# Performance work log

Hardware: AMD Instinct MI355X
Metric: run time of the kernel (lower is better)

Reference implementation:

```python
import jax, jax.numpy as jnp
import numpy as np

B, CH, H, W = 32, 128, 32, 32
EMB = 64      # embedding_dim
NEMB = 8192   # codebook size


def setup_inputs() -> dict:
    key = jax.random.key(0)
    k1, k2, k3, k4 = jax.random.split(key, 4)
    z = jax.random.normal(k1, (B, CH, H, W), jnp.float32)
    # 1x1 conv == per-pixel linear: weight [EMB, CH], bias [EMB]
    proj_w = jax.random.normal(k2, (EMB, CH), jnp.float32) * 0.05
    proj_b = jax.random.normal(k3, (EMB,), jnp.float32) * 0.01
    embed_w = jax.random.normal(k4, (NEMB, EMB), jnp.float32)
    return {"z": z, "proj_w": proj_w, "proj_b": proj_b, "embed_w": embed_w}


def reference(z, proj_w, proj_b, embed_w):
    Bz, C, Hh, Ww = z.shape
    sg = jax.lax.stop_gradient
    # 1x1 conv then permute(0,2,3,1): [B,C,H,W] -> [B,H,W,E]
    z_e = jnp.einsum('bchw,ec->bhwe', z, proj_w) + proj_b
    flat = z_e.reshape(-1, z_e.shape[-1])  # [N, E], N = B*H*W
    dist = ((flat * flat).sum(1, keepdims=True)
            - 2.0 * (flat @ embed_w.T)
            + (embed_w * embed_w).sum(1)[None, :])
    z_q_ind = jnp.argmin(dist, axis=1).reshape(Bz, Hh, Ww)  # argmax(-dist)
    z_q_emb = embed_w[z_q_ind]  # gather: [B,H,W,E]
    commitment_cost = 0.25
    kld_scale = 10.0
    latent_loss = kld_scale * (
        commitment_cost * jnp.mean((sg(z_q_emb) - z_e) ** 2)
        + jnp.mean((z_q_emb - sg(z_e)) ** 2))
    z_q_flat = z_q_emb
    # straight-through estimator
    z_q_st = z_e + sg(z_q_emb - z_e)
    out = jnp.transpose(z_q_st, (0, 3, 1, 2))  # [B,E,H,W]
    return out, z_q_flat, latent_loss, z_q_ind
```

## Files before the change

### kernel.cpp

```cpp
#include <hip/hip_runtime.h>

#define NPIX   32768
#define NEMB_  8192
#define EMB_   64
#define CH_    128
#define CAPP   512

#define OUT_OFF  0
#define ZQ_OFF   2097152
#define LOSS_OFF 4194304
#define IND_OFF  4194305

typedef _Float16 h8   __attribute__((ext_vector_type(8)));
typedef float    f16f __attribute__((ext_vector_type(16)));

__global__ __launch_bounds__(256) void k_wpack(
    const float* __restrict__ ew, float4* __restrict__ W4,
    float* __restrict__ wsq, float* __restrict__ wsqp,
    float* __restrict__ lacc, int* __restrict__ done)
{
    const int tid = threadIdx.x;
    const int m   = blockIdx.x * 256 + tid;
    const float4* wr = (const float4*)(ew + (size_t)m * EMB_);
    float w[EMB_];
    float s = 0.f;
    #pragma unroll
    for (int i = 0; i < 16; i++) {
        float4 v = wr[i];
        w[4*i] = v.x; w[4*i+1] = v.y; w[4*i+2] = v.z; w[4*i+3] = v.w;
        s += v.x*v.x + v.y*v.y + v.z*v.z + v.w*v.w;
    }
    wsq[m] = s;
    float sh = (float)(_Float16)s;
    float sl = s - sh;
    const int t  = m >> 5;
    const int li = m & 31;
    #pragma unroll
    for (int s5 = 0; s5 < 4; s5++) {
        #pragma unroll
        for (int h = 0; h < 2; h++) {
            h8 hh;
            #pragma unroll
            for (int j = 0; j < 8; j++) hh[j] = (_Float16)w[s5 * 16 + h * 8 + j];
            W4[(size_t)(t * 5 + s5) * 64 + h * 32 + li] = __builtin_bit_cast(float4, hh);
        }
    }
    {
        h8 hh;
        #pragma unroll
        for (int j = 0; j < 8; j++) hh[j] = (_Float16)0.f;
        hh[0] = (_Float16)sh; hh[1] = (_Float16)sl;
        W4[(size_t)(t * 5 + 4) * 64 + 0 * 32 + li] = __builtin_bit_cast(float4, hh);
        #pragma unroll
        for (int j = 0; j < 8; j++) hh[j] = (_Float16)0.f;
        W4[(size_t)(t * 5 + 4) * 64 + 1 * 32 + li] = __builtin_bit_cast(float4, hh);
    }
    __shared__ float red[256];
    red[tid] = s;
    __syncthreads();
    for (int o = 128; o > 0; o >>= 1) {
        if (tid < o) red[tid] = fmaxf(red[tid], red[tid + o]);
        __syncthreads();
    }
    if (tid == 0) wsqp[blockIdx.x] = red[0];
    if (blockIdx.x == 0 && tid == 0) { *lacc = 0.f; *done = 0; }
}

__global__ __launch_bounds__(256) void k_proj(
    const float* __restrict__ z, const float* __restrict__ pw,
    const float* __restrict__ pb, float* __restrict__ z_e,
    float* __restrict__ xsq)
{
    __shared__ __align__(16) float wT[CH_ * EMB_];
    __shared__ float xp[4][64];
    const int tid = threadIdx.x;
    for (int i = tid; i < CH_ * EMB_; i += 256) {
        const int c = i >> 6, e = i & 63;
        wT[i] = pw[e * CH_ + c];
    }
    __syncthreads();

    const int px = tid & 63;
    const int eq = tid >> 6;
    const int n  = blockIdx.x * 64 + px;
    const int b  = n >> 10;
    const int hw = n & 1023;
    const float* zp = z + (size_t)b * (CH_ * 1024) + hw;

    float acc[16];
    #pragma unroll
    for (int j = 0; j < 16; j++) acc[j] = 0.f;

    #pragma unroll 4
    for (int c = 0; c < CH_; c++) {
        const float zv = zp[(size_t)c * 1024];
        const float4* wr = (const float4*)(wT + c * EMB_ + eq * 16);
        float4 w0 = wr[0], w1 = wr[1], w2 = wr[2], w3 = wr[3];
        acc[0]  = fmaf(zv, w0.x, acc[0]);  acc[1]  = fmaf(zv, w0.y, acc[1]);
        acc[2]  = fmaf(zv, w0.z, acc[2]);  acc[3]  = fmaf(zv, w0.w, acc[3]);
        acc[4]  = fmaf(zv, w1.x, acc[4]);  acc[5]  = fmaf(zv, w1.y, acc[5]);
        acc[6]  = fmaf(zv, w1.z, acc[6]);  acc[7]  = fmaf(zv, w1.w, acc[7]);
        acc[8]  = fmaf(zv, w2.x, acc[8]);  acc[9]  = fmaf(zv, w2.y, acc[9]);
        acc[10] = fmaf(zv, w2.z, acc[10]); acc[11] = fmaf(zv, w2.w, acc[11]);
        acc[12] = fmaf(zv, w3.x, acc[12]); acc[13] = fmaf(zv, w3.y, acc[13]);
        acc[14] = fmaf(zv, w3.z, acc[14]); acc[15] = fmaf(zv, w3.w, acc[15]);
    }

    const float4* pb4 = (const float4*)(pb + eq * 16);
    float4 b0 = pb4[0], b1 = pb4[1], b2 = pb4[2], b3 = pb4[3];
    float bb[16] = {b0.x,b0.y,b0.z,b0.w, b1.x,b1.y,b1.z,b1.w,
                    b2.x,b2.y,b2.z,b2.w, b3.x,b3.y,b3.z,b3.w};
    float sq = 0.f;
    #pragma unroll
    for (int j = 0; j < 16; j++) { acc[j] += bb[j]; sq += acc[j] * acc[j]; }

    float4* zo = (float4*)(z_e + (size_t)n * EMB_ + eq * 16);
    zo[0] = make_float4(acc[0],  acc[1],  acc[2],  acc[3]);
    zo[1] = make_float4(acc[4],  acc[5],  acc[6],  acc[7]);
    zo[2] = make_float4(acc[8],  acc[9],  acc[10], acc[11]);
    zo[3] = make_float4(acc[12], acc[13], acc[14], acc[15]);
    xp[eq][px] = sq;
    __syncthreads();
    if (tid < 64)
        xsq[blockIdx.x * 64 + tid] = xp[0][tid] + xp[1][tid] + xp[2][tid] + xp[3][tid];
}

__device__ __forceinline__ unsigned long long pack_key(float d, int m)
{
    unsigned fb = __float_as_uint(d);
    fb ^= ((int)fb < 0) ? 0xFFFFFFFFu : 0x80000000u;
    return ((unsigned long long)fb << 32) | (unsigned)m;
}

__global__ __launch_bounds__(256, 2) void k_fused2(
    const float4* __restrict__ W4, const float* __restrict__ z_e,
    const float* __restrict__ xsq, const float* __restrict__ wsqp,
    const float* __restrict__ wsq, const float* __restrict__ ew,
    float* __restrict__ out, float* __restrict__ lacc, int* __restrict__ done)
{
    __shared__ __align__(16) float xs[64][68];
    __shared__ float s1s[512], s2s[512], s3s[512];
    __shared__ short i1s[512], i2s[512];
    __shared__ float thr_s[64];
    __shared__ int   pairs[CAPP];
    __shared__ unsigned long long wbest[4][64];
    __shared__ int   winner_s[64];
    __shared__ int   smask[64];
    __shared__ float lred[256];
    __shared__ int   npair_s;
    __shared__ float wm_s;

    const int tid  = threadIdx.x;
    const int wv   = tid >> 6;
    const int lane = tid & 63;
    const int n0   = blockIdx.x * 64;
    const int hlf  = lane >> 5;

    if (tid == 0) npair_s = 0;
    if (tid < 64) smask[tid] = 0;
    wbest[wv][lane] = ~0ULL;
    if (tid < 32) {
        float w = wsqp[tid];
        #pragma unroll
        for (int o = 16; o > 0; o >>= 1) w = fmaxf(w, __shfl_xor(w, o));
        if (tid == 0) wm_s = w;
    }
    #pragma unroll
    for (int k = 0; k < 4; k++) {
        const int idx = k * 256 + tid;
        const int px = idx >> 4, i = idx & 15;
        ((float4*)&xs[px][0])[i] =
            *(const float4*)(z_e + (size_t)(n0 + px) * EMB_ + i * 4);
    }
    __syncthreads();

    h8 bfr[2][5];
    #pragma unroll
    for (int j = 0; j < 2; j++) {
        const int px = j * 32 + (lane & 31);
        #pragma unroll
        for (int s5 = 0; s5 < 4; s5++) {
            float4 u0 = *(const float4*)(&xs[px][s5 * 16 + hlf * 8]);
            float4 u1 = *(const float4*)(&xs[px][s5 * 16 + hlf * 8 + 4]);
            h8 hh;
            hh[0]=(_Float16)u0.x; hh[1]=(_Float16)u0.y; hh[2]=(_Float16)u0.z; hh[3]=(_Float16)u0.w;
            hh[4]=(_Float16)u1.x; hh[5]=(_Float16)u1.y; hh[6]=(_Float16)u1.z; hh[7]=(_Float16)u1.w;
            bfr[j][s5] = hh;
        }
        h8 hh;
        #pragma unroll
        for (int q = 0; q < 8; q++) hh[q] = (_Float16)0.f;
        if (hlf == 0) { hh[0] = (_Float16)-0.5f; hh[1] = (_Float16)-0.5f; }
        bfr[j][4] = hh;
    }

    const f16f kzero = {0,0,0,0,0,0,0,0,0,0,0,0,0,0,0,0};
    float s1[2], s2[2], s3[2];
    int   i1[2], i2[2];
    #pragma unroll
    for (int j = 0; j < 2; j++) { s1[j]=s2[j]=s3[j]=-3.0e38f; i1[j]=i2[j]=0; }

    const int tb = wv * 64;
    const float4* Wb = W4 + (size_t)tb * 320 + lane;
    float4 A0[5], A1[5];
    #pragma unroll
    for (int s = 0; s < 5; s++) A0[s] = Wb[s * 64];
    #pragma unroll
    for (int s = 0; s < 5; s++) A1[s] = Wb[320 + s * 64];

#define TILE_BODY(AB, TT, PF)                                                  \
    {                                                                          \
        const int gt = tb + (TT);                                              \
        f16f acc[2];                                                           \
        _Pragma("unroll")                                                      \
        for (int j = 0; j < 2; j++)                                            \
            acc[j] = __builtin_amdgcn_mfma_f32_32x32x16_f16(                   \
                __builtin_bit_cast(h8, AB[0]), bfr[j][0], kzero, 0, 0, 0);     \
        _Pragma("unroll")                                                      \
        for (int s = 1; s < 5; s++) {                                          \
            h8 a = __builtin_bit_cast(h8, AB[s]);                              \
            _Pragma("unroll")                                                  \
            for (int j = 0; j < 2; j++)                                        \
                acc[j] = __builtin_amdgcn_mfma_f32_32x32x16_f16(a, bfr[j][s],  \
                                                                acc[j],0,0,0); \
        }                                                                      \
        {                                                                      \
            const int tp = (PF) < 64 ? (PF) : 63;                              \
            const float4* wp = Wb + (size_t)tp * 320;                          \
            _Pragma("unroll")                                                  \
            for (int s = 0; s < 5; s++) AB[s] = wp[s * 64];                    \
        }                                                                      \
        _Pragma("unroll")                                                      \
        for (int j = 0; j < 2; j++) {                                          \
            float t0 = fmaxf(fmaxf(acc[j][0],  acc[j][1]),  acc[j][2]);        \
            float t1 = fmaxf(fmaxf(acc[j][3],  acc[j][4]),  acc[j][5]);        \
            float t2 = fmaxf(fmaxf(acc[j][6],  acc[j][7]),  acc[j][8]);        \
            float t3 = fmaxf(fmaxf(acc[j][9],  acc[j][10]), acc[j][11]);       \
            float t4 = fmaxf(fmaxf(acc[j][12], acc[j][13]), acc[j][14]);       \
            float v  = fmaxf(fmaxf(fmaxf(t0, t1), fmaxf(t2, t3)),              \
                             fmaxf(t4, acc[j][15]));                           \
            v = fmaxf(v, __shfl_xor(v, 32));                                   \
            bool c1 = v > s1[j];                                               \
            bool c2 = v > s2[j];                                               \
            int  cand = c1 ? i1[j] : gt;                                       \
            i2[j] = c2 ? cand : i2[j];                                         \
            s3[j] = fmaxf(fminf(s2[j], v), s3[j]);                             \
            s3[j] = fminf(s3[j], fmaxf(s2[j], v));                             \
            s2[j] = fmaxf(fminf(s1[j], v), fminf(s2[j], fmaxf(s1[j], v)));     \
            i1[j] = c1 ? gt : i1[j];                                           \
            s1[j] = fmaxf(s1[j], v);                                           \
        }                                                                      \
        if (((TT) & 31) == 31) {                                               \
            const int ch = (tb + (TT)) >> 5;                                   \
            if (lane < 32) {                                                   \
                _Pragma("unroll")                                              \
                for (int j = 0; j < 2; j++) {                                  \
                    const int cell = (j * 32 + lane) * 8 + ch;                 \
                    s1s[cell] = s1[j]; s2s[cell] = s2[j]; s3s[cell] = s3[j];   \
                    i1s[cell] = (short)i1[j]; i2s[cell] = (short)i2[j];        \
                }                                                              \
            }                                                                  \
            _Pragma("unroll")                                                  \
            for (int j = 0; j < 2; j++) {                                      \
                s1[j]=s2[j]=s3[j]=-3.0e38f; i1[j]=i2[j]=0;                     \
            }                                                                  \
        }                                                                      \
    }

    for (int tt = 0; tt < 64; tt += 2) {
        TILE_BODY(A0, tt,     tt + 2)
        TILE_BODY(A1, tt + 1, tt + 3)
    }
#undef TILE_BODY
    __syncthreads();

    if (tid < 64) {
        float s1g = s1s[tid * 8];
        #pragma unroll
        for (int c = 1; c < 8; c++) s1g = fmaxf(s1g, s1s[tid * 8 + c]);
        float E = 0.00125f * sqrtf(xsq[n0 + tid] * wm_s) + 1e-5f * wm_s + 3e-4f;
        thr_s[tid] = s1g - 2.0f * E;
    }
    __syncthreads();
    #pragma unroll
    for (int k = 0; k < 2; k++) {
        const int cell = k * 256 + tid;
        const int px = cell >> 3, ch = cell & 7;
        const float th = thr_s[px];
        const float cs1 = s1s[cell], cs2 = s2s[cell], cs3 = s3s[cell];
        if (cs3 >= th) {
            int pos = atomicAdd(&npair_s, 32);
            if (pos + 32 <= CAPP) {
                for (int t = 0; t < 32; t++)
                    pairs[pos + t] = (px << 8) | (ch * 32 + t);
            } else {
                for (int t = 0; t < 32; t++)
                    if (pos + t < CAPP) pairs[pos + t] = -1;
                smask[px] = 1;
            }
        } else {
            if (cs1 >= th) {
                int pos = atomicAdd(&npair_s, 1);
                if (pos < CAPP) pairs[pos] = (px << 8) | (int)i1s[cell];
                else smask[px] = 1;
            }
            if (cs2 >= th) {
                int pos = atomicAdd(&npair_s, 1);
                if (pos < CAPP) pairs[pos] = (px << 8) | (int)i2s[cell];
                else smask[px] = 1;
            }
        }
    }
    __syncthreads();
    const int np = npair_s < CAPP ? npair_s : CAPP;

    const int lg = lane >> 4;
    const int ld = lane & 15;
    for (int i = wv; i < np; i += 4) {
        const int pr = pairs[i];
        if (pr < 0) continue;
        const int p = pr >> 8;
        if (smask[p]) continue;
        const int t = pr & 255;
        const float4* tb4 = (const float4*)(ew + (size_t)t * 2048);
        float4 wq[8];
        #pragma unroll
        for (int q = 0; q < 8; q++) wq[q] = tb4[q * 64 + lane];
        const float4 xq = *(const float4*)(&xs[p][ld * 4]);
        unsigned long long best = ~0ULL;
        #pragma unroll
        for (int q = 0; q < 8; q++) {
            float dp = wq[q].x*xq.x + wq[q].y*xq.y + wq[q].z*xq.z + wq[q].w*xq.w;
            dp += __shfl_xor(dp, 1);
            dp += __shfl_xor(dp, 2);
            dp += __shfl_xor(dp, 4);
            dp += __shfl_xor(dp, 8);
            const int m = t * 32 + q * 4 + lg;
            unsigned long long key = pack_key(fmaf(-2.f, dp, wsq[m]), m);
            best = key < best ? key : best;
        }
        { unsigned long long o = __shfl_xor(best, 16); best = o < best ? o : best; }
        { unsigned long long o = __shfl_xor(best, 32); best = o < best ? o : best; }
        if (lane == 0) {
            unsigned long long cur = wbest[wv][p];
            wbest[wv][p] = best < cur ? best : cur;
        }
    }
    for (int p = wv; p < 64; p += 4) {
        if (!smask[p]) continue;
        const float4 xq = *(const float4*)(&xs[p][ld * 4]);
        unsigned long long bk = ~0ULL;
        for (int t = 0; t < 256; t++) {
            const float4* tb4 = (const float4*)(ew + (size_t)t * 2048);
            #pragma unroll
            for (int q = 0; q < 8; q++) {
                float4 wv4 = tb4[q * 64 + lane];
                float dp = wv4.x*xq.x + wv4.y*xq.y + wv4.z*xq.z + wv4.w*xq.w;
                dp += __shfl_xor(dp, 1);
                dp += __shfl_xor(dp, 2);
                dp += __shfl_xor(dp, 4);
                dp += __shfl_xor(dp, 8);
                const int m = t * 32 + q * 4 + lg;
                unsigned long long key = pack_key(fmaf(-2.f, dp, wsq[m]), m);
                bk = key < bk ? key : bk;
            }
        }
        { unsigned long long o = __shfl_xor(bk, 16); bk = o < bk ? o : bk; }
        { unsigned long long o = __shfl_xor(bk, 32); bk = o < bk ? o : bk; }
        if (lane == 0) {
            unsigned long long cur = wbest[wv][p];
            wbest[wv][p] = bk < cur ? bk : cur;
        }
    }
    __syncthreads();
    if (tid < 64) {
        unsigned long long k0 = wbest[0][tid];
        unsigned long long k1 = wbest[1][tid];
        unsigned long long k2 = wbest[2][tid];
        unsigned long long k3 = wbest[3][tid];
        k0 = k1 < k0 ? k1 : k0;
        k2 = k3 < k2 ? k3 : k2;
        k0 = k2 < k0 ? k2 : k0;
        const int win = (int)(unsigned)(k0 & 0xFFFFFFFFULL);
        winner_s[tid] = win;
        out[IND_OFF + n0 + tid] = (float)win;
    }
    __syncthreads();
    float lsum = 0.f;
    {
        const int px = tid >> 2, sg = tid & 3;
        const int win = winner_s[px];
        const float4* wr = (const float4*)(ew + (size_t)win * EMB_ + sg * 16);
        float4* xr  = (float4*)(&xs[px][sg * 16]);
        float4* zq4 = (float4*)(out + ZQ_OFF + (size_t)(n0 + px) * EMB_ + sg * 16);
        #pragma unroll
        for (int i = 0; i < 4; i++) {
            float4 w4v = wr[i];
            float4 z4  = xr[i];
            float d0 = w4v.x - z4.x, d1 = w4v.y - z4.y;
            float d2 = w4v.z - z4.z, d3 = w4v.w - z4.w;
            lsum += d0*d0 + d1*d1 + d2*d2 + d3*d3;
            xr[i]  = w4v;
            zq4[i] = w4v;
        }
    }
    __syncthreads();
    {
        const int bI  = n0 >> 10;
        const int hw0 = n0 & 1023;
        float* ob = out + OUT_OFF + (size_t)bI * (EMB_ * 1024) + hw0;
        #pragma unroll
        for (int r = 0; r < 16; r++) {
            const int idx = r * 256 + tid;
            const int e = idx >> 6, px = idx & 63;
            ob[(size_t)e * 1024 + px] = xs[px][e];
        }
    }
    lred[tid] = lsum;
    __syncthreads();
    for (int o = 128; o > 0; o >>= 1) {
        if (tid < o) lred[tid] += lred[tid + o];
        __syncthreads();
    }
    if (tid == 0) {
        atomicAdd(lacc, lred[0]);
        __threadfence();
        int old = atomicAdd(done, 1);
        if (old == (int)gridDim.x - 1) {
            float tot = atomicAdd(lacc, 0.0f);
            out[LOSS_OFF] = 12.5f * (tot / 2097152.0f);
        }
    }
}

extern "C" void kernel_launch(void* const* d_in, const int* in_sizes, int n_in,
                              void* d_out, int out_size, void* d_ws, size_t ws_size,
                              hipStream_t stream)
{
    const float* z  = (const float*)d_in[0];
    const float* pw = (const float*)d_in[1];
    const float* pb = (const float*)d_in[2];
    const float* ew = (const float*)d_in[3];
    float* out = (float*)d_out;

    char* ws = (char*)d_ws;
    float4* W4   = (float4*)(ws);
    float*  xsq  = (float*) (ws + 1310720);
    float*  wsq  = (float*) (ws + 1441792);
    float*  wsqp = (float*) (ws + 1474560);
    float*  lacc = (float*) (ws + 1474688);
    int*    done = (int*)   (ws + 1474692);

    float* z_e = out + ZQ_OFF;

    hipLaunchKernelGGL(k_wpack,  dim3(32),  dim3(256), 0, stream,
                       ew, W4, wsq, wsqp, lacc, done);
    hipLaunchKernelGGL(k_proj,   dim3(512), dim3(256), 0, stream,
                       z, pw, pb, z_e, xsq);
    hipLaunchKernelGGL(k_fused2, dim3(512), dim3(256), 0, stream,
                       W4, z_e, xsq, wsqp, wsq, ew, out, lacc, done);
}
```

Baseline: 186.6 us.

## Enlarge fused VQ tile to 128 pixels with 8 waves and pretransposed projection weights

The fused distance/argmin kernel now handles 128 pixels per block with 512 threads. Each wave covers 32 codebook tiles for 4 pixel groups, so every loaded codebook fragment feeds twice as many MFMAs and the per-chunk candidate flush happens once at the end. Per-pixel winners are merged with shared-memory atomicMin, and the loss reduction uses wave shuffles. The projection weight transpose moves into the codebook-pack kernel so k_proj reads pwT directly instead of rebuilding a shared transposed copy in every block. The trade-offs are higher register and LDS use, only 256 blocks (fewer waves to hide latency), and a larger candidate-pair buffer.

```diff
diff --git a/kernel.cpp b/kernel.cpp
--- a/kernel.cpp
+++ b/kernel.cpp
@@ -4,7 +4,7 @@
 #define NEMB_  8192
 #define EMB_   64
 #define CH_    128
-#define CAPP   512
+#define CAPP   768
 
 #define OUT_OFF  0
 #define ZQ_OFF   2097152
@@ -15,12 +15,19 @@
 typedef float    f16f __attribute__((ext_vector_type(16)));
 
 __global__ __launch_bounds__(256) void k_wpack(
-    const float* __restrict__ ew, float4* __restrict__ W4,
+    const float* __restrict__ ew, const float* __restrict__ pw,
+    float4* __restrict__ W4, float* __restrict__ pwT,
     float* __restrict__ wsq, float* __restrict__ wsqp,
     float* __restrict__ lacc, int* __restrict__ done)
 {
     const int tid = threadIdx.x;
-    const int m   = blockIdx.x * 256 + tid;
+    {
+        const int i = blockIdx.x * 256 + tid;
+        const float v = pw[i];
+        const int e = i >> 7, c = i & 127;
+        pwT[c * 64 + e] = v;
+    }
+    const int m = blockIdx.x * 256 + tid;
     const float4* wr = (const float4*)(ew + (size_t)m * EMB_);
     float w[EMB_];
     float s = 0.f;
@@ -67,21 +74,15 @@
 }
 
 __global__ __launch_bounds__(256) void k_proj(
-    const float* __restrict__ z, const float* __restrict__ pw,
+    const float* __restrict__ z, const float* __restrict__ pwT,
     const float* __restrict__ pb, float* __restrict__ z_e,
     float* __restrict__ xsq)
 {
-    __shared__ __align__(16) float wT[CH_ * EMB_];
     __shared__ float xp[4][64];
-    const int tid = threadIdx.x;
-    for (int i = tid; i < CH_ * EMB_; i += 256) {
-        const int c = i >> 6, e = i & 63;
-        wT[i] = pw[e * CH_ + c];
-    }
-    __syncthreads();
-
-    const int px = tid & 63;
-    const int eq = tid >> 6;
+    const int tid  = threadIdx.x;
+    const int px   = tid & 63;
+    const int eqv  = tid >> 6;
+    const int eq16 = __builtin_amdgcn_readfirstlane(eqv << 4);
     const int n  = blockIdx.x * 64 + px;
     const int b  = n >> 10;
     const int hw = n & 1023;
@@ -94,7 +95,7 @@
     #pragma unroll 4
     for (int c = 0; c < CH_; c++) {
         const float zv = zp[(size_t)c * 1024];
-        const float4* wr = (const float4*)(wT + c * EMB_ + eq * 16);
+        const float4* wr = (const float4*)(pwT + c * 64 + eq16);
         float4 w0 = wr[0], w1 = wr[1], w2 = wr[2], w3 = wr[3];
         acc[0]  = fmaf(zv, w0.x, acc[0]);  acc[1]  = fmaf(zv, w0.y, acc[1]);
         acc[2]  = fmaf(zv, w0.z, acc[2]);  acc[3]  = fmaf(zv, w0.w, acc[3]);
@@ -106,7 +107,7 @@
         acc[14] = fmaf(zv, w3.z, acc[14]); acc[15] = fmaf(zv, w3.w, acc[15]);
     }
 
-    const float4* pb4 = (const float4*)(pb + eq * 16);
+    const float4* pb4 = (const float4*)(pb + eq16);
     float4 b0 = pb4[0], b1 = pb4[1], b2 = pb4[2], b3 = pb4[3];
     float bb[16] = {b0.x,b0.y,b0.z,b0.w, b1.x,b1.y,b1.z,b1.w,
                     b2.x,b2.y,b2.z,b2.w, b3.x,b3.y,b3.z,b3.w};
@@ -114,12 +115,12 @@
     #pragma unroll
     for (int j = 0; j < 16; j++) { acc[j] += bb[j]; sq += acc[j] * acc[j]; }
 
-    float4* zo = (float4*)(z_e + (size_t)n * EMB_ + eq * 16);
+    float4* zo = (float4*)(z_e + (size_t)n * EMB_ + eq16);
     zo[0] = make_float4(acc[0],  acc[1],  acc[2],  acc[3]);
     zo[1] = make_float4(acc[4],  acc[5],  acc[6],  acc[7]);
     zo[2] = make_float4(acc[8],  acc[9],  acc[10], acc[11]);
     zo[3] = make_float4(acc[12], acc[13], acc[14], acc[15]);
-    xp[eq][px] = sq;
+    xp[eqv][px] = sq;
     __syncthreads();
     if (tid < 64)
         xsq[blockIdx.x * 64 + tid] = xp[0][tid] + xp[1][tid] + xp[2][tid] + xp[3][tid];
@@ -132,33 +133,32 @@
     return ((unsigned long long)fb << 32) | (unsigned)m;
 }
 
-__global__ __launch_bounds__(256, 2) void k_fused2(
+__global__ __launch_bounds__(512, 2) void k_fused3(
     const float4* __restrict__ W4, const float* __restrict__ z_e,
     const float* __restrict__ xsq, const float* __restrict__ wsqp,
     const float* __restrict__ wsq, const float* __restrict__ ew,
     float* __restrict__ out, float* __restrict__ lacc, int* __restrict__ done)
 {
-    __shared__ __align__(16) float xs[64][68];
-    __shared__ float s1s[512], s2s[512], s3s[512];
-    __shared__ short i1s[512], i2s[512];
-    __shared__ float thr_s[64];
+    __shared__ __align__(16) float xs[128][68];
+    __shared__ float s1s[1024], s2s[1024], s3s[1024];
+    __shared__ short i1s[1024], i2s[1024];
+    __shared__ float thr_s[128];
     __shared__ int   pairs[CAPP];
-    __shared__ unsigned long long wbest[4][64];
-    __shared__ int   winner_s[64];
-    __shared__ int   smask[64];
-    __shared__ float lred[256];
+    __shared__ unsigned long long pbest[128];
+    __shared__ int   winner_s[128];
+    __shared__ int   smask[128];
+    __shared__ float wred[8];
     __shared__ int   npair_s;
     __shared__ float wm_s;
 
     const int tid  = threadIdx.x;
     const int wv   = tid >> 6;
     const int lane = tid & 63;
-    const int n0   = blockIdx.x * 64;
+    const int n0   = blockIdx.x * 128;
     const int hlf  = lane >> 5;
 
     if (tid == 0) npair_s = 0;
-    if (tid < 64) smask[tid] = 0;
-    wbest[wv][lane] = ~0ULL;
+    if (tid < 128) { smask[tid] = 0; pbest[tid] = ~0ULL; }
     if (tid < 32) {
         float w = wsqp[tid];
         #pragma unroll
@@ -167,16 +167,16 @@
     }
     #pragma unroll
     for (int k = 0; k < 4; k++) {
-        const int idx = k * 256 + tid;
+        const int idx = k * 512 + tid;
         const int px = idx >> 4, i = idx & 15;
         ((float4*)&xs[px][0])[i] =
             *(const float4*)(z_e + (size_t)(n0 + px) * EMB_ + i * 4);
     }
     __syncthreads();
 
-    h8 bfr[2][5];
-    #pragma unroll
-    for (int j = 0; j < 2; j++) {
+    h8 bfr[4][5];
+    #pragma unroll
+    for (int j = 0; j < 4; j++) {
         const int px = j * 32 + (lane & 31);
         #pragma unroll
         for (int s5 = 0; s5 < 4; s5++) {
@@ -195,12 +195,12 @@
     }
 
     const f16f kzero = {0,0,0,0,0,0,0,0,0,0,0,0,0,0,0,0};
-    float s1[2], s2[2], s3[2];
-    int   i1[2], i2[2];
-    #pragma unroll
-    for (int j = 0; j < 2; j++) { s1[j]=s2[j]=s3[j]=-3.0e38f; i1[j]=i2[j]=0; }
-
-    const int tb = wv * 64;
+    float s1[4], s2[4], s3[4];
+    int   i1[4], i2[4];
+    #pragma unroll
+    for (int j = 0; j < 4; j++) { s1[j]=s2[j]=s3[j]=-3.0e38f; i1[j]=i2[j]=0; }
+
+    const int tb = wv * 32;
     const float4* Wb = W4 + (size_t)tb * 320 + lane;
     float4 A0[5], A1[5];
     #pragma unroll
@@ -211,27 +211,27 @@
 #define TILE_BODY(AB, TT, PF)                                                  \
     {                                                                          \
         const int gt = tb + (TT);                                              \
-        f16f acc[2];                                                           \
+        f16f acc[4];                                                           \
         _Pragma("unroll")                                                      \
-        for (int j = 0; j < 2; j++)                                            \
+        for (int j = 0; j < 4; j++)                                            \
             acc[j] = __builtin_amdgcn_mfma_f32_32x32x16_f16(                   \
                 __builtin_bit_cast(h8, AB[0]), bfr[j][0], kzero, 0, 0, 0);     \
         _Pragma("unroll")                                                      \
         for (int s = 1; s < 5; s++) {                                          \
             h8 a = __builtin_bit_cast(h8, AB[s]);                              \
             _Pragma("unroll")                                                  \
-            for (int j = 0; j < 2; j++)                                        \
+            for (int j = 0; j < 4; j++)                                        \
                 acc[j] = __builtin_amdgcn_mfma_f32_32x32x16_f16(a, bfr[j][s],  \
                                                                 acc[j],0,0,0); \
         }                                                                      \
         {                                                                      \
-            const int tp = (PF) < 64 ? (PF) : 63;                              \
+            const int tp = (PF) < 32 ? (PF) : 31;                              \
             const float4* wp = Wb + (size_t)tp * 320;                          \
             _Pragma("unroll")                                                  \
             for (int s = 0; s < 5; s++) AB[s] = wp[s * 64];                    \
         }                                                                      \
         _Pragma("unroll")                                                      \
-        for (int j = 0; j < 2; j++) {                                          \
+        for (int j = 0; j < 4; j++) {                                          \
             float t0 = fmaxf(fmaxf(acc[j][0],  acc[j][1]),  acc[j][2]);        \
             float t1 = fmaxf(fmaxf(acc[j][3],  acc[j][4]),  acc[j][5]);        \
             float t2 = fmaxf(fmaxf(acc[j][6],  acc[j][7]),  acc[j][8]);        \
@@ -250,31 +250,25 @@
             i1[j] = c1 ? gt : i1[j];                                           \
             s1[j] = fmaxf(s1[j], v);                                           \
         }                                                                      \
-        if (((TT) & 31) == 31) {                                               \
-            const int ch = (tb + (TT)) >> 5;                                   \
-            if (lane < 32) {                                                   \
-                _Pragma("unroll")                                              \
-                for (int j = 0; j < 2; j++) {                                  \
-                    const int cell = (j * 32 + lane) * 8 + ch;                 \
-                    s1s[cell] = s1[j]; s2s[cell] = s2[j]; s3s[cell] = s3[j];   \
-                    i1s[cell] = (short)i1[j]; i2s[cell] = (short)i2[j];        \
-                }                                                              \
-            }                                                                  \
-            _Pragma("unroll")                                                  \
-            for (int j = 0; j < 2; j++) {                                      \
-                s1[j]=s2[j]=s3[j]=-3.0e38f; i1[j]=i2[j]=0;                     \
-            }                                                                  \
-        }                                                                      \
-    }
-
-    for (int tt = 0; tt < 64; tt += 2) {
+    }
+
+    for (int tt = 0; tt < 32; tt += 2) {
         TILE_BODY(A0, tt,     tt + 2)
         TILE_BODY(A1, tt + 1, tt + 3)
     }
 #undef TILE_BODY
-    __syncthreads();
-
-    if (tid < 64) {
+
+    if (lane < 32) {
+        #pragma unroll
+        for (int j = 0; j < 4; j++) {
+            const int cell = (j * 32 + lane) * 8 + wv;
+            s1s[cell] = s1[j]; s2s[cell] = s2[j]; s3s[cell] = s3[j];
+            i1s[cell] = (short)i1[j]; i2s[cell] = (short)i2[j];
+        }
+    }
+    __syncthreads();
+
+    if (tid < 128) {
         float s1g = s1s[tid * 8];
         #pragma unroll
         for (int c = 1; c < 8; c++) s1g = fmaxf(s1g, s1s[tid * 8 + c]);
@@ -284,7 +278,7 @@
     __syncthreads();
     #pragma unroll
     for (int k = 0; k < 2; k++) {
-        const int cell = k * 256 + tid;
+        const int cell = k * 512 + tid;
         const int px = cell >> 3, ch = cell & 7;
         const float th = thr_s[px];
         const float cs1 = s1s[cell], cs2 = s2s[cell], cs3 = s3s[cell];
@@ -316,7 +310,7 @@
 
     const int lg = lane >> 4;
     const int ld = lane & 15;
-    for (int i = wv; i < np; i += 4) {
+    for (int i = wv; i < np; i += 8) {
         const int pr = pairs[i];
         if (pr < 0) continue;
         const int p = pr >> 8;
@@ -341,12 +335,9 @@
         }
         { unsigned long long o = __shfl_xor(best, 16); best = o < best ? o : best; }
         { unsigned long long o = __shfl_xor(best, 32); best = o < best ? o : best; }
-        if (lane == 0) {
-            unsigned long long cur = wbest[wv][p];
-            wbest[wv][p] = best < cur ? best : cur;
-        }
-    }
-    for (int p = wv; p < 64; p += 4) {
+        if (lane == 0) atomicMin(&pbest[p], best);
+    }
+    for (int p = wv; p < 128; p += 8) {
         if (!smask[p]) continue;
         const float4 xq = *(const float4*)(&xs[p][ld * 4]);
         unsigned long long bk = ~0ULL;
@@ -367,21 +358,11 @@
         }
         { unsigned long long o = __shfl_xor(bk, 16); bk = o < bk ? o : bk; }
         { unsigned long long o = __shfl_xor(bk, 32); bk = o < bk ? o : bk; }
-        if (lane == 0) {
-            unsigned long long cur = wbest[wv][p];
-            wbest[wv][p] = bk < cur ? bk : cur;
-        }
-    }
-    __syncthreads();
-    if (tid < 64) {
-        unsigned long long k0 = wbest[0][tid];
-        unsigned long long k1 = wbest[1][tid];
-        unsigned long long k2 = wbest[2][tid];
-        unsigned long long k3 = wbest[3][tid];
-        k0 = k1 < k0 ? k1 : k0;
-        k2 = k3 < k2 ? k3 : k2;
-        k0 = k2 < k0 ? k2 : k0;
-        const int win = (int)(unsigned)(k0 & 0xFFFFFFFFULL);
+        if (lane == 0) atomicMin(&pbest[p], bk);
+    }
+    __syncthreads();
+    if (tid < 128) {
+        const int win = (int)(unsigned)(pbest[tid] & 0xFFFFFFFFULL);
         winner_s[tid] = win;
         out[IND_OFF + n0 + tid] = (float)win;
     }
@@ -411,19 +392,23 @@
         float* ob = out + OUT_OFF + (size_t)bI * (EMB_ * 1024) + hw0;
         #pragma unroll
         for (int r = 0; r < 16; r++) {
-            const int idx = r * 256 + tid;
-            const int e = idx >> 6, px = idx & 63;
+            const int idx = r * 512 + tid;
+            const int e = idx >> 7, px = idx & 127;
             ob[(size_t)e * 1024 + px] = xs[px][e];
         }
     }
-    lred[tid] = lsum;
-    __syncthreads();
-    for (int o = 128; o > 0; o >>= 1) {
-        if (tid < o) lred[tid] += lred[tid + o];
-        __syncthreads();
-    }
+    {
+        float v = lsum;
+        #pragma unroll
+        for (int o = 1; o < 64; o <<= 1) v += __shfl_xor(v, o);
+        if (lane == 0) wred[wv] = v;
+    }
+    __syncthreads();
     if (tid == 0) {
-        atomicAdd(lacc, lred[0]);
+        float s = wred[0];
+        #pragma unroll
+        for (int k = 1; k < 8; k++) s += wred[k];
+        atomicAdd(lacc, s);
         __threadfence();
         int old = atomicAdd(done, 1);
         if (old == (int)gridDim.x - 1) {
@@ -445,18 +430,19 @@
 
     char* ws = (char*)d_ws;
     float4* W4   = (float4*)(ws);
-    float*  xsq  = (float*) (ws + 1310720);
-    float*  wsq  = (float*) (ws + 1441792);
-    float*  wsqp = (float*) (ws + 1474560);
-    float*  lacc = (float*) (ws + 1474688);
-    int*    done = (int*)   (ws + 1474692);
+    float*  pwT  = (float*) (ws + 1310720);
+    float*  xsq  = (float*) (ws + 1343488);
+    float*  wsq  = (float*) (ws + 1474560);
+    float*  wsqp = (float*) (ws + 1507328);
+    float*  lacc = (float*) (ws + 1507456);
+    int*    done = (int*)   (ws + 1507460);
 
     float* z_e = out + ZQ_OFF;
 
     hipLaunchKernelGGL(k_wpack,  dim3(32),  dim3(256), 0, stream,
-                       ew, W4, wsq, wsqp, lacc, done);
+                       ew, pw, W4, pwT, wsq, wsqp, lacc, done);
     hipLaunchKernelGGL(k_proj,   dim3(512), dim3(256), 0, stream,
-                       z, pw, pb, z_e, xsq);
-    hipLaunchKernelGGL(k_fused2, dim3(512), dim3(256), 0, stream,
+                       z, pwT, pb, z_e, xsq);
+    hipLaunchKernelGGL(k_fused3, dim3(256), dim3(512), 0, stream,
                        W4, z_e, xsq, wsqp, wsq, ew, out, lacc, done);
 }
```

Result: faster. 174.0 us (-6.8%).
